# Performance work log

Hardware: AMD Instinct MI355X
Metric: run time of the kernel (lower is better)

## Reference

```python
import jax, jax.numpy as jnp
import numpy as np
import math

D = 1024
H = 16
DH = D // H
B = 4
NSEQ = 1024
NSEG = 2
EXP = 4


def layer_norm(x, w, b=None, eps=1e-5):
    mu = jnp.mean(x, axis=-1, keepdims=True)
    var = jnp.mean((x - mu) ** 2, axis=-1, keepdims=True)
    y = (x - mu) * jax.lax.rsqrt(var + eps) * w
    return y + b if b is not None else y


def apply_rope(x, positions):
    # x: [B, L, H, Dh]; ESM-style rotate-half RoPE
    dh = x.shape[-1]
    inv_freq = 1.0 / (10000.0 ** (jnp.arange(0, dh, 2, dtype=jnp.float32) / dh))
    freqs = positions.astype(jnp.float32)[:, None] * inv_freq[None, :]  # [L, Dh/2]
    emb = jnp.concatenate([freqs, freqs], axis=-1)  # [L, Dh]
    cos = jnp.cos(emb)[None, :, None, :]
    sin = jnp.sin(emb)[None, :, None, :]
    x1, x2 = jnp.split(x, 2, axis=-1)
    return x * cos + jnp.concatenate([-x2, x1], axis=-1) * sin


def timestep_embedding(timesteps, embedding_dim=256, max_len=10000):
    # timesteps: [N]
    ts = timesteps * max_len
    half = embedding_dim // 2
    emb = math.log(max_len) / (half - 1)
    freqs = jnp.exp(jnp.arange(half, dtype=jnp.float32) * -emb)
    e = ts.astype(jnp.float32)[:, None] * freqs[None, :]
    return jnp.concatenate([jnp.sin(e), jnp.cos(e)], axis=1)  # [N, 256]


def make_autoregressive_attn_mask(batch_mask, n_seg):
    b, n_res = batch_mask.shape
    L = (n_seg + 1) * n_res
    causal = jnp.tril(jnp.ones((L, L), dtype=bool))[None, None]  # [1,1,L,L]
    tiled = jnp.tile(batch_mask, (1, n_seg + 1)).astype(bool)  # [B, L]
    key_valid = tiled[:, None, None, :]
    q_valid = tiled[:, None, :, None]
    allowed = causal & key_valid & q_valid  # [B,1,L,L]
    first_edit = (batch_mask[:, None, :] * batch_mask[:, :, None]).astype(bool)
    allowed = allowed.at[:, 0, :n_res, :n_res].set(first_edit)
    return allowed


def setup_inputs() -> dict:
    key = jax.random.key(0)
    ks = jax.random.split(key, 32)
    s = 0.02
    p = lambda i, shape: jax.random.normal(ks[i], shape, dtype=jnp.float32) * s
    inp = {
        'x_seq': jax.random.normal(ks[0], (B, NSEQ, D), dtype=jnp.float32),
        'x_struc': jax.random.normal(ks[1], (B, 1, D), dtype=jnp.float32),
        'temp': jax.random.uniform(ks[2], (B, 1, 1), dtype=jnp.float32),
        'mask': jnp.ones((B, NSEQ), dtype=jnp.float32),
        'ln_qs_w': jnp.ones((D,), jnp.float32), 'ln_qs_b': jnp.zeros((D,), jnp.float32),
        'W_qkv_seq': p(3, (D, 3 * D)),
        'ln_qt_w': jnp.ones((D,), jnp.float32), 'ln_qt_b': jnp.zeros((D,), jnp.float32),
        'W_qkv_struc': p(4, (D, 3 * D)),
        'q_ln_seq_w': jnp.ones((D,), jnp.float32), 'k_ln_seq_w': jnp.ones((D,), jnp.float32),
        'q_ln_struc_w': jnp.ones((D,), jnp.float32), 'k_ln_struc_w': jnp.ones((D,), jnp.float32),
        'W_out_seq': p(5, (D, D)), 'W_out_struc': p(6, (D, D)),
        'temp_w1': p(7, (1, D)), 'temp_b1': jnp.zeros((D,), jnp.float32),
        'temp_w2': p(8, (D, D)), 'temp_b2': jnp.zeros((D,), jnp.float32),
        'T_w1': p(9, (256, D)), 'T_b1': jnp.zeros((D,), jnp.float32),
        'T_w2': p(10, (D, D)), 'T_b2': jnp.zeros((D,), jnp.float32),
        'ffn_seq_ln_w': jnp.ones((D,), jnp.float32), 'ffn_seq_ln_b': jnp.zeros((D,), jnp.float32),
        'ffn_seq_w1': p(11, (D, EXP * D)), 'ffn_seq_w2': p(12, (EXP * D, D)),
        'ffn_struc_ln_w': jnp.ones((D,), jnp.float32), 'ffn_struc_ln_b': jnp.zeros((D,), jnp.float32),
        'ffn_struc_w1': p(13, (D, EXP * D)), 'ffn_struc_w2': p(14, (EXP * D, D)),
        'T': 1,
    }
    return inp


def reference(x_seq, x_struc, temp, mask,
              ln_qs_w, ln_qs_b, W_qkv_seq,
              ln_qt_w, ln_qt_b, W_qkv_struc,
              q_ln_seq_w, k_ln_seq_w, q_ln_struc_w, k_ln_struc_w,
              W_out_seq, W_out_struc,
              temp_w1, temp_b1, temp_w2, temp_b2,
              T_w1, T_b1, T_w2, T_b2,
              ffn_seq_ln_w, ffn_seq_ln_b, ffn_seq_w1, ffn_seq_w2,
              ffn_struc_ln_w, ffn_struc_ln_b, ffn_struc_w1, ffn_struc_w2,
              T):
    b, n_seq, d = x_seq.shape
    n_seg, index = NSEG, 0  # index=0 prefill path

    # --- seq track QKV (index == 0 only) ---
    qkv_seq = layer_norm(x_seq, ln_qs_w, ln_qs_b) @ W_qkv_seq
    q_s, k_s, v_s = jnp.split(qkv_seq, 3, axis=-1)
    q_s = layer_norm(q_s, q_ln_seq_w)
    k_s = layer_norm(k_s, k_ln_seq_w)
    pos_seq = jnp.arange(n_seq)
    q_s = apply_rope(q_s.reshape(b, n_seq, H, DH), pos_seq).reshape(b, n_seq, d)
    k_s = apply_rope(k_s.reshape(b, n_seq, H, DH), pos_seq).reshape(b, n_seq, d)

    # --- struc track conditioning + QKV ---
    position_T = jnp.arange(n_seg, dtype=jnp.float32) * T / 100.0
    T_input = jnp.repeat(position_T, n_seq)[index:index + 1]  # [1]
    x_norm = layer_norm(x_struc, ln_qt_w, ln_qt_b)
    temp_e = jax.nn.silu(temp @ temp_w1 + temp_b1) @ temp_w2 + temp_b2  # [B,1,D]
    t_emb = timestep_embedding(T_input)  # [1,256]
    T_e = jax.nn.silu(t_emb @ T_w1 + T_b1) @ T_w2 + T_b2  # [1,D]
    x_mod = x_norm + temp_e + T_e[None, :, :]
    qkv_t = x_mod @ W_qkv_struc
    q_t, k_t, v_t = jnp.split(qkv_t, 3, axis=-1)
    q_t = layer_norm(q_t, q_ln_struc_w)
    k_t = layer_norm(k_t, k_ln_struc_w)
    pos_res = jnp.tile(jnp.arange(n_seq), n_seg)[index:index + 1]  # [1]
    q_t = apply_rope(q_t.reshape(b, 1, H, DH), pos_res).reshape(b, 1, d)
    k_t = apply_rope(k_t.reshape(b, 1, H, DH), pos_res).reshape(b, 1, d)

    # --- KV cache contents for index 0: [seq tokens, struc token] ---
    keys = jnp.concatenate([k_s, k_t], axis=1)    # [B, N_seq+1, D]
    values = jnp.concatenate([v_s, v_t], axis=1)
    queries = jnp.concatenate([q_s, q_t], axis=1)

    to_heads = lambda t: t.reshape(b, -1, H, DH).transpose(0, 2, 1, 3)  # b h s d
    qh, kh, vh = to_heads(queries), to_heads(keys), to_heads(values)

    allowed = make_autoregressive_attn_mask(mask, n_seg)  # [B,1,L,L]
    Lq = n_seq + index + 1
    attn_mask = allowed[:, :, :Lq, :Lq]

    scale = 1.0 / math.sqrt(DH)
    scores = jnp.einsum('bhqd,bhkd->bhqk', qh, kh) * scale
    scores = jnp.where(attn_mask, scores, -1e9)
    probs = jax.nn.softmax(scores, axis=-1)
    ctx = jnp.einsum('bhqk,bhkd->bhqd', probs, vh)
    ctx = ctx.transpose(0, 2, 1, 3).reshape(b, Lq, d)

    out_seq = ctx[:, :n_seq] @ W_out_seq
    out_struc = ctx[:, n_seq:] @ W_out_struc

    # residuals (scaling_factor = 1)
    x_seq = x_seq + out_seq
    x_struc = x_struc + out_struc

    # GELU FFNs (LN -> Linear -> GELU -> Linear, no bias)
    h_seq = jax.nn.gelu(layer_norm(x_seq, ffn_seq_ln_w, ffn_seq_ln_b) @ ffn_seq_w1, approximate=False) @ ffn_seq_w2
    x_seq = x_seq + h_seq
    h_struc = jax.nn.gelu(layer_norm(x_struc, ffn_struc_ln_w, ffn_struc_ln_b) @ ffn_struc_w1, approximate=False) @ ffn_struc_w2
    x_struc = x_struc + h_struc

    return (x_seq, x_struc)
```

## Files before the change

### kernel.cpp

```cpp
#include <hip/hip_runtime.h>

typedef __attribute__((ext_vector_type(8))) short short8;
typedef __attribute__((ext_vector_type(4))) float f32x4;
typedef __attribute__((ext_vector_type(4))) unsigned short us4;

#define DEV static __device__ __forceinline__

DEV float bf2f(unsigned short u){ union{unsigned u; float f;} v; v.u=((unsigned)u)<<16; return v.f; }
DEV unsigned short f2bf(float f){ union{float f; unsigned u;} v; v.f=f; unsigned r=v.u+0x7fffu+((v.u>>16)&1u); return (unsigned short)(r>>16); }
DEV float gelu_f(float x){ return 0.5f*x*(1.0f+erff(x*0.7071067811865475f)); }
DEV float silu_f(float x){ return x/(1.0f+__expf(-x)); }

DEV void gload16(const void* g, void* l){
  __builtin_amdgcn_global_load_lds((const __attribute__((address_space(1))) void*)g,
                                   (__attribute__((address_space(3))) void*)l, 16, 0, 0);
}

DEV void blk_reduce2(float &a, float &b){
  #pragma unroll
  for (int off=32; off>0; off>>=1){ a += __shfl_down(a,off); b += __shfl_down(b,off); }
  __shared__ float sa[4], sb[4];
  int w=threadIdx.x>>6;
  if((threadIdx.x&63)==0){ sa[w]=a; sb[w]=b; }
  __syncthreads();
  a=sa[0]+sa[1]+sa[2]+sa[3]; b=sb[0]+sb[1]+sb[2]+sb[3];
}

template<int OUTF32>
__global__ __launch_bounds__(256) void ln_rows(const float* __restrict__ x,
    const float* __restrict__ w, const float* __restrict__ bias, void* __restrict__ outp)
{
  int row=blockIdx.x, t=threadIdx.x;
  const float* xr = x + (size_t)row*1024;
  float4 v = *(const float4*)(xr + t*4);
  float s=v.x+v.y+v.z+v.w;
  float s2=v.x*v.x+v.y*v.y+v.z*v.z+v.w*v.w;
  blk_reduce2(s,s2);
  float mu=s*(1.0f/1024.0f);
  float rs=rsqrtf(s2*(1.0f/1024.0f)-mu*mu+1e-5f);
  int d0=t*4;
  const float* vp=(const float*)&v;
  float y[4];
  #pragma unroll
  for(int j=0;j<4;j++){ float bb = bias? bias[d0+j] : 0.0f; y[j]=(vp[j]-mu)*rs*w[d0+j]+bb; }
  if (OUTF32){
    float4 o; o.x=y[0];o.y=y[1];o.z=y[2];o.w=y[3];
    *(float4*)((float*)outp + (size_t)row*1024 + d0) = o;
  } else {
    us4 o;
    #pragma unroll
    for(int j=0;j<4;j++) o[j]=f2bf(y[j]);
    *(us4*)((unsigned short*)outp + (size_t)row*1024 + d0) = o;
  }
}

__global__ __launch_bounds__(256) void wtrans(const float* __restrict__ Bm,
    unsigned short* __restrict__ Bt, int K, int N)
{
  __shared__ float tile[32][33];
  int nb = blockIdx.x*32, kb = blockIdx.y*32;
  int tx = threadIdx.x&31, ty = threadIdx.x>>5;
  #pragma unroll
  for(int i=0;i<32;i+=8) tile[ty+i][tx] = Bm[(size_t)(kb+ty+i)*N + nb+tx];
  __syncthreads();
  #pragma unroll
  for(int i=0;i<32;i+=8) Bt[(size_t)(nb+ty+i)*K + kb+tx] = f2bf(tile[tx][ty+i]);
}

__global__ __launch_bounds__(256) void vtrans(const unsigned short* __restrict__ qkv,
    unsigned short* __restrict__ vT)
{
  __shared__ unsigned short tile[32][33];
  int d0 = blockIdx.x*32, tk0 = blockIdx.y*32, b = blockIdx.z;
  int tx = threadIdx.x&31, ty = threadIdx.x>>5;
  #pragma unroll
  for(int i=0;i<32;i+=8) tile[ty+i][tx] = qkv[(size_t)(b*1024+tk0+ty+i)*3072 + 2048 + d0+tx];
  __syncthreads();
  #pragma unroll
  for(int i=0;i<32;i+=8) vT[(size_t)(b*1024+d0+ty+i)*1024 + tk0+tx] = tile[tx][ty+i];
}

__global__ void rope_table(float* __restrict__ tab){
  int idx = blockIdx.x*256 + threadIdx.x;
  if (idx >= 1024*32) return;
  int pos = idx>>5, i = idx&31;
  float inv = exp2f(-(float)i * (13.287712379549449f/32.0f));
  float a = (float)pos*inv;
  tab[idx*2]   = cosf(a);
  tab[idx*2+1] = sinf(a);
}

__global__ __launch_bounds__(256) void qk_ln_rope(
    const unsigned short* __restrict__ qkv, const float* __restrict__ qw, const float* __restrict__ kw,
    const float* __restrict__ tab, unsigned short* __restrict__ qr, unsigned short* __restrict__ kr)
{
  __shared__ float lnr[1024];
  int row=blockIdx.x, part=blockIdx.y, t=threadIdx.x;
  const unsigned short* src = qkv + (size_t)row*3072 + part*1024 + t*4;
  us4 u = *(const us4*)src;
  float x[4];
  #pragma unroll
  for(int j=0;j<4;j++) x[j]=bf2f(u[j]);
  float s=x[0]+x[1]+x[2]+x[3];
  float s2=x[0]*x[0]+x[1]*x[1]+x[2]*x[2]+x[3]*x[3];
  blk_reduce2(s,s2);
  float mu=s*(1.0f/1024.0f);
  float rsg=rsqrtf(s2*(1.0f/1024.0f)-mu*mu+1e-5f);
  const float* w = part? kw : qw;
  int d0=t*4;
  #pragma unroll
  for(int j=0;j<4;j++) lnr[d0+j]=(x[j]-mu)*rsg*w[d0+j];
  __syncthreads();
  int n = row & 1023;
  unsigned short* dst = (part? kr: qr) + (size_t)row*1024 + d0;
  us4 o;
  #pragma unroll
  for(int j=0;j<4;j++){
    int d=d0+j, dh=d&63, fi=dh&31;
    float c=tab[(n*32+fi)*2], sn=tab[(n*32+fi)*2+1];
    float p=lnr[d^32];
    o[j]=f2bf(lnr[d]*c + ((dh<32)? -p : p)*sn);
  }
  *(us4*)dst = o;
}

template<int EPI>
__global__ __launch_bounds__(512) void gemm256(
    const unsigned short* __restrict__ A, int lda,
    const unsigned short* __restrict__ Bt, int ldb,
    int N, int K, void* Cout)
{
  __shared__ unsigned short As[16384];
  __shared__ unsigned short Bs[16384];
  const int t=threadIdx.x;
  int GX=gridDim.x, GY=gridDim.y, nwg=GX*GY;
  int bx, by;
  if (!(nwg&7)){
    int d = blockIdx.y*GX + blockIdx.x;
    int g = (d&7)*(nwg>>3) + (d>>3);
    bx = g%GX; by = g/GX;
  } else { bx = blockIdx.x; by = blockIdx.y; }
  const int m0=by*256, n0=bx*256;
  const int l=t&63, w=t>>6, lg=l>>4, lr=l&15;
  const int wr=w>>2, wc=w&3;
  const int srow=t>>3, sseg=(t&7)^((t>>3)&7);
  const f32x4 z4 = {0.f,0.f,0.f,0.f};
  f32x4 acc[8][4];
  #pragma unroll
  for(int i=0;i<8;i++)
    #pragma unroll
    for(int j=0;j<4;j++) acc[i][j]=z4;
  for (int k0=0;k0<K;k0+=64){
    __syncthreads();
    #pragma unroll
    for(int i=0;i<4;i++){
      gload16(A  + (size_t)(m0+srow+i*64)*lda + k0 + sseg*8, As + i*4096 + w*512);
      gload16(Bt + (size_t)(n0+srow+i*64)*ldb + k0 + sseg*8, Bs + i*4096 + w*512);
    }
    __syncthreads();
    #pragma unroll
    for(int ks=0;ks<2;ks++){
      short8 a[8], bfr[4];
      #pragma unroll
      for(int m=0;m<8;m++){
        int row=wr*128+m*16+lr;
        a[m] = *(const short8*)&As[row*64 + ((ks*4+lg)^(row&7))*8];
      }
      #pragma unroll
      for(int n=0;n<4;n++){
        int row=wc*64+n*16+lr;
        bfr[n] = *(const short8*)&Bs[row*64 + ((ks*4+lg)^(row&7))*8];
      }
      #pragma unroll
      for(int m=0;m<8;m++)
        #pragma unroll
        for(int n=0;n<4;n++)
          acc[m][n] = __builtin_amdgcn_mfma_f32_16x16x32_bf16(a[m], bfr[n], acc[m][n], 0,0,0);
    }
  }
  #pragma unroll
  for(int m=0;m<8;m++){
    #pragma unroll
    for(int n=0;n<4;n++){
      #pragma unroll
      for(int r=0;r<4;r++){
        int row=m0+wr*128+m*16+lg*4+r, col=n0+wc*64+n*16+lr;
        size_t idx=(size_t)row*N+col;
        float v=acc[m][n][r];
        if (EPI==2){ ((unsigned short*)Cout)[idx] = f2bf(gelu_f(v)); }
        else { ((unsigned short*)Cout)[idx] = f2bf(v); }
      }
    }
  }
}

template<int EPI>
__global__ __launch_bounds__(256) void gemm_bt(
    const unsigned short* __restrict__ A, int lda,
    const unsigned short* __restrict__ Bt, int ldb,
    int N, int K, void* Cout, const float* resp, void* Cout2)
{
  __shared__ unsigned short As[8192];
  __shared__ unsigned short Bs[8192];
  const int t=threadIdx.x;
  int GX=gridDim.x, GY=gridDim.y, nwg=GX*GY;
  int m0, n0;
  if (!((GX&7) || (nwg&63))){
    int d = blockIdx.y*GX + blockIdx.x;
    int xcd = d&7, j = d>>3;
    int g = xcd*(nwg>>3) + j;
    int chunk = g>>6, local = g&63;
    int chunks_x = GX>>3;
    int cx = chunk%chunks_x, cy = chunk/chunks_x;
    n0 = (cx*8 + (local&7))*128;
    m0 = (cy*8 + (local>>3))*128;
  } else {
    m0 = blockIdx.y*128; n0 = blockIdx.x*128;
  }
  const int kofs = blockIdx.z*K;
  unsigned short* Cb = (unsigned short*)(blockIdx.z ? Cout2 : Cout);
  const int l=t&63, w=t>>6, lg=l>>4, lr=l&15;
  const int wm=(w>>1)*64, wn=(w&1)*64;
  const int srow=t>>3, sseg=(t&7)^(srow&7);
  const f32x4 z4 = {0.f,0.f,0.f,0.f};
  f32x4 acc[4][4];
  #pragma unroll
  for(int i=0;i<4;i++)
    #pragma unroll
    for(int j=0;j<4;j++) acc[i][j]=z4;
  for (int k0=0;k0<K;k0+=64){
    __syncthreads();
    #pragma unroll
    for(int i=0;i<4;i++){
      gload16(A  + (size_t)(m0+srow+i*32)*lda + kofs + k0 + sseg*8, As + w*512 + i*2048);
      gload16(Bt + (size_t)(n0+srow+i*32)*ldb + kofs + k0 + sseg*8, Bs + w*512 + i*2048);
    }
    __syncthreads();
    #pragma unroll
    for(int ks=0;ks<2;ks++){
      short8 a[4], bfr[4];
      #pragma unroll
      for(int m=0;m<4;m++){
        int row=wm+m*16+lr;
        a[m] = *(const short8*)&As[row*64 + ((ks*4+lg)^(row&7))*8];
      }
      #pragma unroll
      for(int n=0;n<4;n++){
        int row=wn+n*16+lr;
        bfr[n] = *(const short8*)&Bs[row*64 + ((ks*4+lg)^(row&7))*8];
      }
      #pragma unroll
      for(int m=0;m<4;m++)
        #pragma unroll
        for(int n=0;n<4;n++)
          acc[m][n] = __builtin_amdgcn_mfma_f32_16x16x32_bf16(a[m], bfr[n], acc[m][n], 0,0,0);
    }
  }
  #pragma unroll
  for(int m=0;m<4;m++){
    #pragma unroll
    for(int n=0;n<4;n++){
      #pragma unroll
      for(int r=0;r<4;r++){
        int row=m0+wm+m*16+lg*4+r, col=n0+wn+n*16+lr;
        size_t idx=(size_t)row*N+col;
        float v=acc[m][n][r];
        if (EPI==1){ ((float*)Cout)[idx] = v + resp[idx]; }
        else if (EPI==2){ ((unsigned short*)Cout)[idx] = f2bf(gelu_f(v)); }
        else { Cb[idx] = f2bf(v); }
      }
    }
  }
}

__global__ __launch_bounds__(256) void comb2(float* __restrict__ out,
    const unsigned short* __restrict__ p0, const unsigned short* __restrict__ p1)
{
  size_t i = ((size_t)blockIdx.x*256 + threadIdx.x)*4;
  us4 a = *(const us4*)(p0+i);
  us4 b = *(const us4*)(p1+i);
  float4 o = *(float4*)(out+i);
  o.x += bf2f(a[0])+bf2f(b[0]);
  o.y += bf2f(a[1])+bf2f(b[1]);
  o.z += bf2f(a[2])+bf2f(b[2]);
  o.w += bf2f(a[3])+bf2f(b[3]);
  *(float4*)(out+i) = o;
}

__global__ __launch_bounds__(256) void flash_seq(
    const unsigned short* __restrict__ qr, const unsigned short* __restrict__ kr,
    const unsigned short* __restrict__ vT, unsigned short* __restrict__ ctx)
{
  __shared__ unsigned short Pl[4][32][64];
  const int t=threadIdx.x, w=t>>6, l=t&63, lg=l>>4, lr=l&15;
  int d = blockIdx.y*gridDim.x + blockIdx.x;
  int xcd = d&7;
  int g = xcd*64 + (d>>3);
  const int bh = g>>3, b = bh>>4, h = bh&15;
  const int q0 = (g&7)*128;
  const f32x4 z4 = {0.f,0.f,0.f,0.f};
  short8 qf[2][2];
  #pragma unroll
  for(int mf=0;mf<2;mf++)
    #pragma unroll
    for(int ks=0;ks<2;ks++)
      qf[mf][ks] = *(const short8*)(qr + (size_t)(b*1024 + q0 + w*32 + mf*16 + lr)*1024 + h*64 + ks*32 + lg*8);
  short8 ones;
  #pragma unroll
  for(int j=0;j<8;j++) ones[j] = (short)0x3F80;
  f32x4 o[2][4], lacc[2];
  #pragma unroll
  for(int mf=0;mf<2;mf++){
    lacc[mf]=z4;
    #pragma unroll
    for(int nd=0;nd<4;nd++) o[mf][nd]=z4;
  }
  for (int kv0=0;kv0<1024;kv0+=64){
    f32x4 s[2][4];
    #pragma unroll
    for(int mf=0;mf<2;mf++)
      #pragma unroll
      for(int nf=0;nf<4;nf++) s[mf][nf]=z4;
    #pragma unroll
    for(int ks=0;ks<2;ks++){
      #pragma unroll
      for(int nf=0;nf<4;nf++){
        short8 kf = *(const short8*)(kr + (size_t)(b*1024+kv0+nf*16+lr)*1024 + h*64 + ks*32 + lg*8);
        s[0][nf] = __builtin_amdgcn_mfma_f32_16x16x32_bf16(qf[0][ks], kf, s[0][nf],0,0,0);
        s[1][nf] = __builtin_amdgcn_mfma_f32_16x16x32_bf16(qf[1][ks], kf, s[1][nf],0,0,0);
      }
    }
    #pragma unroll
    for(int mf=0;mf<2;mf++)
      #pragma unroll
      for(int nf=0;nf<4;nf++)
        #pragma unroll
        for(int r=0;r<4;r++)
          s[mf][nf][r] = __expf(fmaf(s[mf][nf][r], 0.125f, -8.0f));
    #pragma unroll
    for(int mf=0;mf<2;mf++)
      #pragma unroll
      for(int nf=0;nf<4;nf++)
        #pragma unroll
        for(int r=0;r<4;r++){
          int prow = mf*16+lg*4+r;
          int col = (((nf*2+(lr>>3)) ^ (prow&7))<<3) + (lr&7);
          Pl[w][prow][col] = f2bf(s[mf][nf][r]);
        }
    #pragma unroll
    for(int ks2=0;ks2<2;ks2++){
      short8 pa0 = *(const short8*)&Pl[w][lr]   [((ks2*4+lg)^(lr&7))<<3];
      short8 pa1 = *(const short8*)&Pl[w][16+lr][((ks2*4+lg)^(lr&7))<<3];
      lacc[0] = __builtin_amdgcn_mfma_f32_16x16x32_bf16(pa0, ones, lacc[0],0,0,0);
      lacc[1] = __builtin_amdgcn_mfma_f32_16x16x32_bf16(pa1, ones, lacc[1],0,0,0);
      #pragma unroll
      for(int nd=0;nd<4;nd++){
        short8 vf = *(const short8*)(vT + (size_t)(b*1024 + h*64 + nd*16+lr)*1024 + kv0 + ks2*32 + lg*8);
        o[0][nd] = __builtin_amdgcn_mfma_f32_16x16x32_bf16(pa0, vf, o[0][nd],0,0,0);
        o[1][nd] = __builtin_amdgcn_mfma_f32_16x16x32_bf16(pa1, vf, o[1][nd],0,0,0);
      }
    }
  }
  #pragma unroll
  for(int mf=0;mf<2;mf++){
    #pragma unroll
    for(int r=0;r<4;r++){
      float inv = 1.0f/lacc[mf][r];
      #pragma unroll
      for(int nd=0;nd<4;nd++){
        ctx[(size_t)(b*1024 + q0 + w*32 + mf*16 + lg*4 + r)*1024 + h*64 + nd*16 + lr]
          = f2bf(o[mf][nd][r]*inv);
      }
    }
  }
}

__global__ __launch_bounds__(256) void struc_prep_a(const float* __restrict__ T_w1, float* __restrict__ sTacc){
  int j = blockIdx.x*256+threadIdx.x;
  float u=0.f;
  #pragma unroll
  for(int i=0;i<16;i++) u += T_w1[(size_t)(128+blockIdx.y*16+i)*1024 + j];
  atomicAdd(&sTacc[j], u);
}

__global__ __launch_bounds__(256) void struc_prep_b(const float* __restrict__ temp,
    const float* __restrict__ temp_w1, const float* __restrict__ temp_b1,
    const float* __restrict__ T_b1, const float* __restrict__ sTacc,
    float* __restrict__ sT, float* __restrict__ stemp)
{
  int j = blockIdx.x*256+threadIdx.x;
  sT[j] = silu_f(sTacc[j]+T_b1[j]);
  #pragma unroll
  for(int b=0;b<4;b++){ float z = temp[b]*temp_w1[j]+temp_b1[j]; stemp[b*1024+j]=silu_f(z); }
}

__global__ __launch_bounds__(256) void struc_xmod(const float* __restrict__ xs,
    const float* __restrict__ qtw, const float* __restrict__ qtb,
    const float* __restrict__ eacc, const float* __restrict__ tacc,
    const float* __restrict__ temp_b2, const float* __restrict__ T_b2, float* __restrict__ xmod)
{
  int b=blockIdx.x, t=threadIdx.x;
  float4 v = *(const float4*)(xs + (size_t)b*1024 + t*4);
  float s=v.x+v.y+v.z+v.w, s2=v.x*v.x+v.y*v.y+v.z*v.z+v.w*v.w;
  blk_reduce2(s,s2);
  float mu=s*(1.0f/1024.0f);
  float rs=rsqrtf(s2*(1.0f/1024.0f)-mu*mu+1e-5f);
  const float* vp=(const float*)&v;
  #pragma unroll
  for(int j=0;j<4;j++){
    int d=t*4+j;
    xmod[b*1024+d] = (vp[j]-mu)*rs*qtw[d] + qtb[d] + eacc[b*1024+d] + tacc[d] + T_b2[d] + temp_b2[d];
  }
}

template<int MR>
__global__ __launch_bounds__(256) void smallm_part(
    const float* __restrict__ A, const float* __restrict__ Bm,
    float* __restrict__ accp, int K, int N)
{
  __shared__ float As[MR][64];
  const int t=threadIdx.x;
  const int n = blockIdx.x*256 + t;
  const int k0 = blockIdx.y*64;
  if (t < MR*64){ int m=t>>6, kk=t&63; As[m][kk]=A[(size_t)m*K + k0+kk]; }
  __syncthreads();
  float acc[MR];
  #pragma unroll
  for(int m=0;m<MR;m++) acc[m]=0.f;
  #pragma unroll 8
  for(int kk=0;kk<64;kk++){
    float wv = Bm[(size_t)(k0+kk)*N + n];
    #pragma unroll
    for(int m=0;m<MR;m++) acc[m] += As[m][kk]*wv;
  }
  #pragma unroll
  for(int m=0;m<MR;m++) atomicAdd(&accp[(size_t)m*N + n], acc[m]);
}

__global__ __launch_bounds__(256) void gelu_vec(const float* __restrict__ in, float* __restrict__ out, int n){
  int i = blockIdx.x*256+threadIdx.x;
  if (i<n) out[i]=gelu_f(in[i]);
}

__global__ __launch_bounds__(256) void struc_qk_ln(float* qkv_t,
    const float* __restrict__ qw, const float* __restrict__ kw)
{
  int b=blockIdx.x>>1, part=blockIdx.x&1, t=threadIdx.x;
  float* xr = qkv_t + (size_t)b*3072 + part*1024;
  float4 v = *(const float4*)(xr + t*4);
  float s=v.x+v.y+v.z+v.w, s2=v.x*v.x+v.y*v.y+v.z*v.z+v.w*v.w;
  blk_reduce2(s,s2);
  float mu=s*(1.0f/1024.0f);
  float rsg=rsqrtf(s2*(1.0f/1024.0f)-mu*mu+1e-5f);
  const float* w = part? kw : qw;
  const float* vp=(const float*)&v;
  #pragma unroll
  for(int j=0;j<4;j++) xr[t*4+j]=(vp[j]-mu)*rsg*w[t*4+j];
}

__global__ __launch_bounds__(256) void struc_attn_part(
    const float* __restrict__ qkv_t, const unsigned short* __restrict__ kr,
    const unsigned short* __restrict__ qkv, float* __restrict__ part)
{
  __shared__ float qs[64];
  __shared__ float pb[4][64];
  const int bh=blockIdx.x, b=bh>>4, h=bh&15;
  const int t=threadIdx.x, w=t>>6, l=t&63;
  if (t<64) qs[t]=qkv_t[(size_t)b*3072 + h*64 + t];
  __syncthreads();
  const int key = blockIdx.y*256 + w*64 + l;
  const unsigned short* krow = kr + (size_t)(b*1024+key)*1024 + h*64;
  float s=0.f;
  #pragma unroll
  for(int j=0;j<8;j++){
    short8 kk = *(const short8*)(krow + j*8);
    #pragma unroll
    for(int e=0;e<8;e++) s += qs[j*8+e]*bf2f((unsigned short)kk[e]);
  }
  s *= 0.125f;
  float mx=s;
  #pragma unroll
  for(int off=32;off>0;off>>=1) mx=fmaxf(mx,__shfl_xor(mx,off));
  float p=__expf(s-mx);
  float ls=p;
  #pragma unroll
  for(int off=32;off>0;off>>=1) ls+=__shfl_xor(ls,off);
  pb[w][l]=p;
  const int k0 = blockIdx.y*256 + w*64;
  float cacc=0.f;
  for(int k2=0;k2<64;k2++)
    cacc += pb[w][k2]*bf2f(qkv[(size_t)(b*1024+k0+k2)*3072 + 2048 + h*64 + l]);
  float* pp = part + ((size_t)bh*16 + blockIdx.y*4 + w)*66;
  if(l==0){ pp[0]=mx; pp[1]=ls; }
  pp[2+l]=cacc;
}

__global__ __launch_bounds__(64) void struc_attn_comb(
    const float* __restrict__ part, const float* __restrict__ qkv_t, float* __restrict__ ctx_t)
{
  const int bh=blockIdx.x, b=bh>>4, h=bh&15, l=threadIdx.x;
  float M=-1e30f;
  #pragma unroll
  for(int i=0;i<16;i++) M=fmaxf(M, part[((size_t)bh*16+i)*66]);
  float lsum=0.f, cacc=0.f;
  #pragma unroll
  for(int i=0;i<16;i++){
    const float* pp = part + ((size_t)bh*16+i)*66;
    float f=__expf(pp[0]-M);
    lsum += pp[1]*f;
    cacc += pp[2+l]*f;
  }
  float qd=qkv_t[(size_t)b*3072 + h*64 + l];
  float kd=qkv_t[(size_t)b*3072 + 1024 + h*64 + l];
  float prod=qd*kd;
  #pragma unroll
  for(int off=32;off>0;off>>=1) prod+=__shfl_xor(prod,off);
  float st=prod*0.125f;
  float M2=fmaxf(M,st), fA=__expf(M-M2), pt=__expf(st-M2);
  cacc = cacc*fA + pt*qkv_t[(size_t)b*3072 + 2048 + h*64 + l];
  lsum = lsum*fA + pt;
  ctx_t[(size_t)b*1024 + h*64 + l] = cacc/lsum;
}

extern "C" void kernel_launch(void* const* d_in, const int* in_sizes, int n_in,
                              void* d_out, int out_size, void* d_ws, size_t ws_size,
                              hipStream_t stream){
  const float* x_seq    = (const float*)d_in[0];
  const float* x_struc  = (const float*)d_in[1];
  const float* temp     = (const float*)d_in[2];
  const float* ln_qs_w  = (const float*)d_in[4];
  const float* ln_qs_b  = (const float*)d_in[5];
  const float* W_qkv_seq= (const float*)d_in[6];
  const float* ln_qt_w  = (const float*)d_in[7];
  const float* ln_qt_b  = (const float*)d_in[8];
  const float* W_qkv_st = (const float*)d_in[9];
  const float* q_ln_seq_w=(const float*)d_in[10];
  const float* k_ln_seq_w=(const float*)d_in[11];
  const float* q_ln_st_w= (const float*)d_in[12];
  const float* k_ln_st_w= (const float*)d_in[13];
  const float* W_out_seq= (const float*)d_in[14];
  const float* W_out_st = (const float*)d_in[15];
  const float* temp_w1  = (const float*)d_in[16];
  const float* temp_b1  = (const float*)d_in[17];
  const float* temp_w2  = (const float*)d_in[18];
  const float* temp_b2  = (const float*)d_in[19];
  const float* T_w1     = (const float*)d_in[20];
  const float* T_b1     = (const float*)d_in[21];
  const float* T_w2     = (const float*)d_in[22];
  const float* T_b2     = (const float*)d_in[23];
  const float* ffn_s_ln_w=(const float*)d_in[24];
  const float* ffn_s_ln_b=(const float*)d_in[25];
  const float* ffn_s_w1 = (const float*)d_in[26];
  const float* ffn_s_w2 = (const float*)d_in[27];
  const float* ffn_t_ln_w=(const float*)d_in[28];
  const float* ffn_t_ln_b=(const float*)d_in[29];
  const float* ffn_t_w1 = (const float*)d_in[30];
  const float* ffn_t_w2 = (const float*)d_in[31];

  char* ws = (char*)d_ws;
  unsigned short* xn   = (unsigned short*)(ws + 0);
  unsigned short* qkv  = (unsigned short*)(ws + 8388608);
  unsigned short* qr   = (unsigned short*)(ws + 33554432);
  unsigned short* kr   = (unsigned short*)(ws + 41943040);
  unsigned short* ctx  = (unsigned short*)(ws + 50331648);
  float* tab   = (float*)(ws + 58720256);
  char* sm = ws + 58982400;
  float* sT    = (float*)(sm + 0);
  float* stemp = (float*)(sm + 4096);
  float* tacc  = (float*)(sm + 20544);
  float* eacc  = (float*)(sm + 24640);
  float* xmod  = (float*)(sm + 41024);
  float* qkvt  = (float*)(sm + 57408);
  float* ctxt  = (float*)(sm + 106560);
  float* xsn   = (float*)(sm + 122944);
  float* hs    = (float*)(sm + 139328);
  float* hsacc = (float*)(sm + 204864);
  float* part  = (float*)(sm + 270400);
  float* sTacc = (float*)(sm + 540800);
  unsigned short* wqkvT = (unsigned short*)(ws + 50331648);
  unsigned short* woutT = (unsigned short*)(ws + 33554432);
  unsigned short* ffn1T = (unsigned short*)(ws + 41943040);
  unsigned short* ffn2T = (unsigned short*)(ws + 50331648);
  unsigned short* vT    = xn;
  unsigned short* hbuf  = qkv;
  unsigned short* pbuf0 = xn;
  unsigned short* pbuf1 = kr;
  float* outf = (float*)d_out;
  float* out_tail = outf + 4194304;

  ln_rows<0><<<4096,256,0,stream>>>(x_seq, ln_qs_w, ln_qs_b, xn);
  wtrans<<<dim3(96,32),256,0,stream>>>(W_qkv_seq, wqkvT, 1024, 3072);
  rope_table<<<128,256,0,stream>>>(tab);
  gemm256<0><<<dim3(12,16),512,0,stream>>>(xn, 1024, wqkvT, 1024, 3072, 1024, qkv);
  vtrans<<<dim3(32,32,4),256,0,stream>>>(qkv, vT);
  qk_ln_rope<<<dim3(4096,2),256,0,stream>>>(qkv, q_ln_seq_w, k_ln_seq_w, tab, qr, kr);
  flash_seq<<<dim3(8,64),256,0,stream>>>(qr, kr, vT, ctx);
  hipMemsetAsync(sTacc, 0, 1024*4, stream);
  hipMemsetAsync(tacc, 0, 1024*4, stream);
  hipMemsetAsync(eacc, 0, 4096*4, stream);
  hipMemsetAsync(qkvt, 0, 12288*4, stream);
  struc_prep_a<<<dim3(4,8),256,0,stream>>>(T_w1, sTacc);
  struc_prep_b<<<4,256,0,stream>>>(temp, temp_w1, temp_b1, T_b1, sTacc, sT, stemp);
  smallm_part<1><<<dim3(4,16),256,0,stream>>>(sT, T_w2, tacc, 1024, 1024);
  smallm_part<4><<<dim3(4,16),256,0,stream>>>(stemp, temp_w2, eacc, 1024, 1024);
  struc_xmod<<<4,256,0,stream>>>(x_struc, ln_qt_w, ln_qt_b, eacc, tacc, temp_b2, T_b2, xmod);
  smallm_part<4><<<dim3(12,16),256,0,stream>>>(xmod, W_qkv_st, qkvt, 1024, 3072);
  struc_qk_ln<<<8,256,0,stream>>>(qkvt, q_ln_st_w, k_ln_st_w);
  struc_attn_part<<<dim3(64,4),256,0,stream>>>(qkvt, kr, qkv, part);
  struc_attn_comb<<<64,64,0,stream>>>(part, qkvt, ctxt);
  wtrans<<<dim3(32,32),256,0,stream>>>(W_out_seq, woutT, 1024, 1024);
  gemm_bt<1><<<dim3(8,32),256,0,stream>>>(ctx, 1024, woutT, 1024, 1024, 1024, outf, x_seq, nullptr);
  hipMemcpyAsync(out_tail, x_struc, 4096*4, hipMemcpyDeviceToDevice, stream);
  smallm_part<4><<<dim3(4,16),256,0,stream>>>(ctxt, W_out_st, out_tail, 1024, 1024);
  ln_rows<0><<<4096,256,0,stream>>>(outf, ffn_s_ln_w, ffn_s_ln_b, xn);
  wtrans<<<dim3(128,32),256,0,stream>>>(ffn_s_w1, ffn1T, 1024, 4096);
  gemm256<2><<<dim3(16,16),512,0,stream>>>(xn, 1024, ffn1T, 1024, 4096, 1024, hbuf);
  wtrans<<<dim3(32,128),256,0,stream>>>(ffn_s_w2, ffn2T, 4096, 1024);
  gemm_bt<0><<<dim3(8,32,2),256,0,stream>>>(hbuf, 4096, ffn2T, 4096, 1024, 2048, pbuf0, nullptr, pbuf1);
  comb2<<<4096,256,0,stream>>>(outf, pbuf0, pbuf1);
  ln_rows<1><<<4,256,0,stream>>>(out_tail, ffn_t_ln_w, ffn_t_ln_b, xsn);
  hipMemsetAsync(hsacc, 0, 16384*4, stream);
  smallm_part<4><<<dim3(16,16),256,0,stream>>>(xsn, ffn_t_w1, hsacc, 1024, 4096);
  gelu_vec<<<64,256,0,stream>>>(hsacc, hs, 16384);
  smallm_part<4><<<dim3(4,64),256,0,stream>>>(hs, ffn_t_w2, out_tail, 4096, 1024);
  (void)in_sizes; (void)n_in; (void)out_size; (void)ws_size;
}
```

Before: 426.3 us.

## Split sequence flash attention over key halves and combine partial outputs

The sequence attention kernel now splits the key range into two halves along a new grid dimension, doubling the block count from 512 to 1024. Each half writes unnormalised bf16 partial outputs and row sums, and a new combine kernel adds them and normalises. The exp is rewritten as exp2 with prescaled constants, and the struc attention reads V from the transposed buffer with vector loads. The split adds an extra pass through global memory and a kernel launch, and rounds the partial outputs to bf16 before they are combined.

```diff
diff --git a/kernel.cpp b/kernel.cpp
--- a/kernel.cpp
+++ b/kernel.cpp
@@ -289,7 +289,8 @@
 
 __global__ __launch_bounds__(256) void flash_seq(
     const unsigned short* __restrict__ qr, const unsigned short* __restrict__ kr,
-    const unsigned short* __restrict__ vT, unsigned short* __restrict__ ctx)
+    const unsigned short* __restrict__ vT,
+    unsigned short* __restrict__ opart, float* __restrict__ lpart)
 {
   __shared__ unsigned short Pl[4][32][64];
   const int t=threadIdx.x, w=t>>6, l=t&63, lg=l>>4, lr=l&15;
@@ -298,6 +299,9 @@
   int g = xcd*64 + (d>>3);
   const int bh = g>>3, b = bh>>4, h = bh&15;
   const int q0 = (g&7)*128;
+  const int half = blockIdx.z;
+  unsigned short* op = opart + (size_t)half*4194304;
+  float* lp = lpart + (size_t)half*65536;
   const f32x4 z4 = {0.f,0.f,0.f,0.f};
   short8 qf[2][2];
   #pragma unroll
@@ -315,7 +319,7 @@
     #pragma unroll
     for(int nd=0;nd<4;nd++) o[mf][nd]=z4;
   }
-  for (int kv0=0;kv0<1024;kv0+=64){
+  for (int kv0=half*512; kv0<half*512+512; kv0+=64){
     f32x4 s[2][4];
     #pragma unroll
     for(int mf=0;mf<2;mf++)
@@ -336,7 +340,7 @@
       for(int nf=0;nf<4;nf++)
         #pragma unroll
         for(int r=0;r<4;r++)
-          s[mf][nf][r] = __expf(fmaf(s[mf][nf][r], 0.125f, -8.0f));
+          s[mf][nf][r] = exp2f(fmaf(s[mf][nf][r], 0.18033688011112043f, -11.541560327111707f));
     #pragma unroll
     for(int mf=0;mf<2;mf++)
       #pragma unroll
@@ -365,14 +369,30 @@
   for(int mf=0;mf<2;mf++){
     #pragma unroll
     for(int r=0;r<4;r++){
-      float inv = 1.0f/lacc[mf][r];
-      #pragma unroll
-      for(int nd=0;nd<4;nd++){
-        ctx[(size_t)(b*1024 + q0 + w*32 + mf*16 + lg*4 + r)*1024 + h*64 + nd*16 + lr]
-          = f2bf(o[mf][nd][r]*inv);
-      }
-    }
-  }
+      int row = b*1024 + q0 + w*32 + mf*16 + lg*4 + r;
+      if (lr==0) lp[(size_t)row*16 + h] = lacc[mf][r];
+      #pragma unroll
+      for(int nd=0;nd<4;nd++)
+        op[(size_t)row*1024 + h*64 + nd*16 + lr] = f2bf(o[mf][nd][r]);
+    }
+  }
+}
+
+__global__ __launch_bounds__(256) void comb_attn2(
+    const unsigned short* __restrict__ o0, const unsigned short* __restrict__ o1,
+    const float* __restrict__ l0, const float* __restrict__ l1,
+    unsigned short* __restrict__ ctx)
+{
+  int row = blockIdx.x, t = threadIdx.x;
+  int d0 = t*4, h = d0>>6;
+  float inv = 1.0f/(l0[(size_t)row*16+h] + l1[(size_t)row*16+h]);
+  size_t i = (size_t)row*1024 + d0;
+  us4 a = *(const us4*)(o0+i);
+  us4 b = *(const us4*)(o1+i);
+  us4 o;
+  #pragma unroll
+  for(int j=0;j<4;j++) o[j] = f2bf((bf2f(a[j])+bf2f(b[j]))*inv);
+  *(us4*)(ctx+i) = o;
 }
 
 __global__ __launch_bounds__(256) void struc_prep_a(const float* __restrict__ T_w1, float* __restrict__ sTacc){
@@ -460,7 +480,7 @@
 
 __global__ __launch_bounds__(256) void struc_attn_part(
     const float* __restrict__ qkv_t, const unsigned short* __restrict__ kr,
-    const unsigned short* __restrict__ qkv, float* __restrict__ part)
+    const unsigned short* __restrict__ vT, float* __restrict__ part)
 {
   __shared__ float qs[64];
   __shared__ float pb[4][64];
@@ -488,8 +508,12 @@
   pb[w][l]=p;
   const int k0 = blockIdx.y*256 + w*64;
   float cacc=0.f;
-  for(int k2=0;k2<64;k2++)
-    cacc += pb[w][k2]*bf2f(qkv[(size_t)(b*1024+k0+k2)*3072 + 2048 + h*64 + l]);
+  #pragma unroll
+  for(int j=0;j<8;j++){
+    short8 vv = *(const short8*)(vT + (size_t)(b*1024 + h*64 + l)*1024 + k0 + j*8);
+    #pragma unroll
+    for(int e=0;e<8;e++) cacc += pb[w][j*8+e]*bf2f((unsigned short)vv[e]);
+  }
   float* pp = part + ((size_t)bh*16 + blockIdx.y*4 + w)*66;
   if(l==0){ pp[0]=mx; pp[1]=ls; }
   pp[2+l]=cacc;
@@ -582,6 +606,8 @@
   unsigned short* ffn1T = (unsigned short*)(ws + 41943040);
   unsigned short* ffn2T = (unsigned short*)(ws + 50331648);
   unsigned short* vT    = xn;
+  unsigned short* opart = qkv;
+  float* lpart          = (float*)(ws + 8388608 + 16777216);
   unsigned short* hbuf  = qkv;
   unsigned short* pbuf0 = xn;
   unsigned short* pbuf1 = kr;
@@ -594,7 +620,8 @@
   gemm256<0><<<dim3(12,16),512,0,stream>>>(xn, 1024, wqkvT, 1024, 3072, 1024, qkv);
   vtrans<<<dim3(32,32,4),256,0,stream>>>(qkv, vT);
   qk_ln_rope<<<dim3(4096,2),256,0,stream>>>(qkv, q_ln_seq_w, k_ln_seq_w, tab, qr, kr);
-  flash_seq<<<dim3(8,64),256,0,stream>>>(qr, kr, vT, ctx);
+  flash_seq<<<dim3(8,64,2),256,0,stream>>>(qr, kr, vT, opart, lpart);
+  comb_attn2<<<4096,256,0,stream>>>(opart, opart+4194304, lpart, lpart+65536, ctx);
   hipMemsetAsync(sTacc, 0, 1024*4, stream);
   hipMemsetAsync(tacc, 0, 1024*4, stream);
   hipMemsetAsync(eacc, 0, 4096*4, stream);
@@ -606,7 +633,7 @@
   struc_xmod<<<4,256,0,stream>>>(x_struc, ln_qt_w, ln_qt_b, eacc, tacc, temp_b2, T_b2, xmod);
   smallm_part<4><<<dim3(12,16),256,0,stream>>>(xmod, W_qkv_st, qkvt, 1024, 3072);
   struc_qk_ln<<<8,256,0,stream>>>(qkvt, q_ln_st_w, k_ln_st_w);
-  struc_attn_part<<<dim3(64,4),256,0,stream>>>(qkvt, kr, qkv, part);
+  struc_attn_part<<<dim3(64,4),256,0,stream>>>(qkvt, kr, vT, part);
   struc_attn_comb<<<64,64,0,stream>>>(part, qkvt, ctxt);
   wtrans<<<dim3(32,32),256,0,stream>>>(W_out_seq, woutT, 1024, 1024);
   gemm_bt<1><<<dim3(8,32),256,0,stream>>>(ctx, 1024, woutT, 1024, 1024, 1024, outf, x_seq, nullptr);
```

After: 430.6 us. No clear change (+1.0%).
